# Performance work log

Hardware: AMD Instinct MI355X
Metric: run time of the kernel (lower is better)

## Reference

```python
import jax, jax.numpy as jnp
import numpy as np

B, H, L, DK = 8, 8, 512, 64
LK, C = 512, 5


def setup_inputs() -> dict:
    key = jax.random.key(0)
    ks = jax.random.split(key, 6)
    d_in = LK * H * DK  # l_k * d_model
    return {
        "Q": jax.random.normal(ks[0], (B, H, L, DK), dtype=jnp.float32),
        "K": jax.random.normal(ks[1], (B, H, LK, DK), dtype=jnp.float32),
        # scale by 1/sqrt(fan_in) so softmax inputs are sane
        "W_proj": jax.random.normal(ks[2], (d_in, C), dtype=jnp.float32) / np.sqrt(d_in),
        "b_proj": jnp.zeros((C,), dtype=jnp.float32),
        "W_q": jax.random.normal(ks[3], (C, C), dtype=jnp.float32) / np.sqrt(C),
        "b_q": jnp.zeros((C,), dtype=jnp.float32),
        "W_k": jax.random.normal(ks[4], (C, C), dtype=jnp.float32) / np.sqrt(C),
        "b_k": jnp.zeros((C,), dtype=jnp.float32),
    }


def reference(Q, K, W_proj, b_proj, W_q, b_q, W_k, b_k):
    b, h, l, d_k = Q.shape
    l_k = K.shape[2]
    n_clusters = b_proj.shape[0]
    hd = h * d_k

    # cluster projections over flattened K
    ck_proj = K.reshape(b, -1) @ W_proj + b_proj            # (b, C)
    cluster_q = jax.nn.softmax(ck_proj @ W_q + b_q, axis=-1)  # (b, C)
    cluster_k = jax.nn.softmax(ck_proj @ W_k + b_k, axis=-1)  # (b, C)

    # Gaussian likelihood term (torch.std is unbiased -> ddof=1)
    mu = jnp.mean(cluster_q, axis=0)                         # (C,)
    sigma = jax.nn.softplus(jnp.std(cluster_k, axis=0, ddof=1))
    log_prob = (-0.5 * ((cluster_k - mu) / sigma) ** 2
                - jnp.log(sigma) - 0.5 * jnp.log(2.0 * jnp.pi))
    # CrossEntropyLoss with prob targets: mean_b(-sum target*log_softmax(input))
    ce = jnp.mean(-jnp.sum(cluster_q * jax.nn.log_softmax(cluster_q, axis=-1), axis=-1))
    loss = -jnp.mean(log_prob) + ce

    # cluster assignment per batch element
    inds = jnp.argmax(cluster_q, axis=-1)                    # (b,) in [0, C)

    # The original per-cluster loop with where(K_cluster != i+1, K_inds, 0) then
    # mean(dim=0)[0] reduces to: mean over batch of K_re[:,0,:] masked where
    # assignment != i+1, broadcast across l_k.
    K_re = K.reshape(b, l_k, hd)
    row0 = K_re[:, 0, :]                                     # (b, hd)
    keep = (inds[None, :] != (jnp.arange(n_clusters) + 1)[:, None]).astype(Q.dtype)  # (C, b)
    means = (keep @ row0) / b                                # (C, hd)

    # broadcast to (b, C, l_k, hd) then raw reshape to (b, h, C, l_k, d_k)
    cm = jnp.broadcast_to(means[None, :, None, :], (b, n_clusters, l_k, hd))
    cm = cm.reshape(b, h, n_clusters, l_k, d_k)

    scale = 1.0 / np.sqrt(d_k)
    scores_qk = jnp.einsum('bhqd,bhkd->bhqk', Q, K) * scale          # (b,h,l,l_k)
    scores_qc = jnp.einsum('bhqd,bhckd->bhcqk', Q, cm) * scale       # (b,h,C,l,l_k)
    # max over cat([qk, qc], dim=2) == elementwise max of qk and max_c qc
    final_score = jnp.maximum(scores_qk, jnp.max(scores_qc, axis=2))
    return final_score, loss
```

## Files before the change

### kernel.cpp

```cpp
#include <hip/hip_runtime.h>
#include <math.h>

#define NB 8
#define NH 8
#define SEQ 512
#define DK 64
#define NC 5
#define D_IN 262144
#define OUT_SCORE (NB*NH*SEQ*SEQ)

typedef short short8 __attribute__((ext_vector_type(8)));
typedef float f32x16 __attribute__((ext_vector_type(16)));

__device__ __forceinline__ short f2bf(float f) {
  unsigned u = __float_as_uint(f);
  u += 0x7fffu + ((u >> 16) & 1u);
  return (short)(u >> 16);
}
__device__ __forceinline__ short8 pack8(float4 a, float4 b) {
  short8 r;
  r[0] = f2bf(a.x); r[1] = f2bf(a.y); r[2] = f2bf(a.z); r[3] = f2bf(a.w);
  r[4] = f2bf(b.x); r[5] = f2bf(b.y); r[6] = f2bf(b.z); r[7] = f2bf(b.w);
  return r;
}

__global__ __launch_bounds__(256) void proj_kernel(const float* __restrict__ K,
                                                   const float* __restrict__ Wp,
                                                   float* __restrict__ ck) {
  int i4 = blockIdx.x * 256 + threadIdx.x;
  const float4* Wp4 = (const float4*)Wp;
  float w[20];
#pragma unroll
  for (int t = 0; t < 5; ++t) {
    float4 v = Wp4[i4 * 5 + t];
    w[4*t+0] = v.x; w[4*t+1] = v.y; w[4*t+2] = v.z; w[4*t+3] = v.w;
  }
  float acc[NB][NC];
#pragma unroll
  for (int b = 0; b < NB; ++b)
#pragma unroll
    for (int c = 0; c < NC; ++c) acc[b][c] = 0.f;
#pragma unroll
  for (int b = 0; b < NB; ++b) {
    float4 kv = ((const float4*)(K + (size_t)b * D_IN))[i4];
    float ke[4] = {kv.x, kv.y, kv.z, kv.w};
#pragma unroll
    for (int e = 0; e < 4; ++e)
#pragma unroll
      for (int c = 0; c < NC; ++c)
        acc[b][c] = fmaf(ke[e], w[5*e + c], acc[b][c]);
  }

  __shared__ float red[4][NB * NC];
  int wave = threadIdx.x >> 6;
  int lane = threadIdx.x & 63;
#pragma unroll
  for (int bc = 0; bc < NB * NC; ++bc) {
    float v = acc[bc / NC][bc % NC];
#pragma unroll
    for (int off = 32; off > 0; off >>= 1) v += __shfl_down(v, off);
    if (lane == 0) red[wave][bc] = v;
  }
  __syncthreads();
  if (threadIdx.x < NB * NC) {
    float s = red[0][threadIdx.x] + red[1][threadIdx.x] +
              red[2][threadIdx.x] + red[3][threadIdx.x];
    atomicAdd(&ck[threadIdx.x], s);
  }
}

__global__ __launch_bounds__(256) void small_kernel(
    const float* __restrict__ K, const float* __restrict__ ck_raw,
    const float* __restrict__ bp, const float* __restrict__ Wq,
    const float* __restrict__ bq, const float* __restrict__ Wk,
    const float* __restrict__ bk, float* __restrict__ means,
    float* __restrict__ loss_out) {
  __shared__ float cq[NB][NC], ckk[NB][NC], ce_sh[NB];
  __shared__ int inds[NB];
  int t = threadIdx.x;
  if (t < NB) {
    float cp[NC], zq[NC], zk[NC];
#pragma unroll
    for (int c = 0; c < NC; ++c) cp[c] = ck_raw[t * NC + c] + bp[c];
#pragma unroll
    for (int c = 0; c < NC; ++c) { zq[c] = bq[c]; zk[c] = bk[c]; }
#pragma unroll
    for (int j = 0; j < NC; ++j)
#pragma unroll
      for (int c = 0; c < NC; ++c) {
        zq[c] = fmaf(cp[j], Wq[j * NC + c], zq[c]);
        zk[c] = fmaf(cp[j], Wk[j * NC + c], zk[c]);
      }
    float m = zq[0];
#pragma unroll
    for (int c = 1; c < NC; ++c) m = fmaxf(m, zq[c]);
    float e[NC], s = 0.f;
#pragma unroll
    for (int c = 0; c < NC; ++c) { e[c] = expf(zq[c] - m); s += e[c]; }
    float inv = 1.f / s;
    float p[NC];
#pragma unroll
    for (int c = 0; c < NC; ++c) { p[c] = e[c] * inv; cq[t][c] = p[c]; }
    int am = 0; float bv = p[0];
#pragma unroll
    for (int c = 1; c < NC; ++c) if (p[c] > bv) { bv = p[c]; am = c; }
    inds[t] = am;
    float se = 0.f;
#pragma unroll
    for (int c = 0; c < NC; ++c) se += expf(p[c] - bv);
    float lse = bv + logf(se);
    float ceb = 0.f;
#pragma unroll
    for (int c = 0; c < NC; ++c) ceb -= p[c] * (p[c] - lse);
    ce_sh[t] = ceb;
    m = zk[0];
#pragma unroll
    for (int c = 1; c < NC; ++c) m = fmaxf(m, zk[c]);
    s = 0.f;
#pragma unroll
    for (int c = 0; c < NC; ++c) { e[c] = expf(zk[c] - m); s += e[c]; }
    inv = 1.f / s;
#pragma unroll
    for (int c = 0; c < NC; ++c) ckk[t][c] = e[c] * inv;
  }
  __syncthreads();
  if (t == 0) {
    float mu[NC];
#pragma unroll
    for (int c = 0; c < NC; ++c) {
      float sm = 0.f;
      for (int b = 0; b < NB; ++b) sm += cq[b][c];
      mu[c] = sm * 0.125f;
    }
    float loss_lp = 0.f;
#pragma unroll
    for (int c = 0; c < NC; ++c) {
      float sm = 0.f;
      for (int b = 0; b < NB; ++b) sm += ckk[b][c];
      float mk = sm * 0.125f;
      float var = 0.f;
      for (int b = 0; b < NB; ++b) {
        float d = ckk[b][c] - mk;
        var += d * d;
      }
      var *= (1.f / 7.f);
      float sd = sqrtf(var);
      float sigma = log1pf(expf(sd));
      float ls = logf(sigma);
      for (int b = 0; b < NB; ++b) {
        float z = (ckk[b][c] - mu[c]) / sigma;
        loss_lp += -0.5f * z * z - ls - 0.91893853320467274f;
      }
    }
    float ce = 0.f;
    for (int b = 0; b < NB; ++b) ce += ce_sh[b];
    ce *= 0.125f;
    loss_out[0] = -(loss_lp / 40.f) + ce;
  }
  __syncthreads();
  for (int idx = t; idx < NC * 512; idx += 256) {
    int c = idx >> 9, j = idx & 511;
    float sm = 0.f;
#pragma unroll
    for (int b = 0; b < NB; ++b)
      if (inds[b] != c + 1) sm += K[(size_t)b * D_IN + j];
    means[idx] = sm * 0.125f;
  }
}

#define LDSTRIDE 72
__global__ __launch_bounds__(256) void score_kernel(const float* __restrict__ Q,
                                                    const float* __restrict__ K,
                                                    const float* __restrict__ means,
                                                    float* __restrict__ out) {
  __shared__ short Qs[128 * LDSTRIDE];
  __shared__ short Ks[128 * LDSTRIDE];

  const int bh = blockIdx.x;
  const int h  = bh & 7;
  const int qblk = blockIdx.y << 7;
  const int kblk = blockIdx.z << 7;
  const int tid = threadIdx.x;
  const int w = tid >> 6, lane = tid & 63;
  const int lo5 = lane & 31, hi = lane >> 5;
  const int wq = (w >> 1) << 6;
  const int wk = (w & 1) << 6;

  const float* Qg = Q + (size_t)bh * (SEQ * DK) + (size_t)qblk * DK;
  const float* Kg = K + (size_t)bh * (SEQ * DK) + (size_t)kblk * DK;

#pragma unroll
  for (int i = 0; i < 4; ++i) {
    int f8 = i * 256 + tid;
    int row = f8 >> 3, c8 = f8 & 7;
    const float4* qp = (const float4*)(Qg + row * DK + c8 * 8);
    const float4* kp = (const float4*)(Kg + row * DK + c8 * 8);
    *(short8*)&Qs[row * LDSTRIDE + c8 * 8] = pack8(qp[0], qp[1]);
    *(short8*)&Ks[row * LDSTRIDE + c8 * 8] = pack8(kp[0], kp[1]);
  }

  const int cmin = (5 * h) >> 3;
  const int cmax = (5 * h + 4) >> 3;
  short8 mfrag[4];
#pragma unroll
  for (int s = 0; s < 4; ++s) {
    float4 a = {0.f, 0.f, 0.f, 0.f}, b = {0.f, 0.f, 0.f, 0.f};
    if (lo5 < 16) {
      int c = (lo5 < 8) ? cmin : cmax;
      const float* mp = means + c * 512 + (lo5 & 7) * 64 + s * 16 + hi * 8;
      a = *(const float4*)mp;
      b = *(const float4*)(mp + 4);
    }
    mfrag[s] = pack8(a, b);
  }

  __syncthreads();

  f32x16 zero;
#pragma unroll
  for (int x = 0; x < 16; ++x) zero[x] = 0.f;

  f32x16 acc00 = zero, acc01 = zero, acc10 = zero, acc11 = zero;
  f32x16 aq0 = zero, aq1 = zero;
#pragma unroll
  for (int s = 0; s < 4; ++s) {
    int co = s * 16 + hi * 8;
    short8 a0 = *(const short8*)&Qs[(wq + lo5)      * LDSTRIDE + co];
    short8 a1 = *(const short8*)&Qs[(wq + 32 + lo5) * LDSTRIDE + co];
    short8 b0 = *(const short8*)&Ks[(wk + lo5)      * LDSTRIDE + co];
    short8 b1 = *(const short8*)&Ks[(wk + 32 + lo5) * LDSTRIDE + co];
    acc00 = __builtin_amdgcn_mfma_f32_32x32x16_bf16(a0, b0, acc00, 0, 0, 0);
    acc01 = __builtin_amdgcn_mfma_f32_32x32x16_bf16(a0, b1, acc01, 0, 0, 0);
    acc10 = __builtin_amdgcn_mfma_f32_32x32x16_bf16(a1, b0, acc10, 0, 0, 0);
    acc11 = __builtin_amdgcn_mfma_f32_32x32x16_bf16(a1, b1, acc11, 0, 0, 0);
    aq0   = __builtin_amdgcn_mfma_f32_32x32x16_bf16(a0, mfrag[s], aq0, 0, 0, 0);
    aq1   = __builtin_amdgcn_mfma_f32_32x32x16_bf16(a1, mfrag[s], aq1, 0, 0, 0);
  }

  float qcv0[16], qcv1[16];
  const int src0 = (hi << 5) + (lo5 & 7);
#pragma unroll
  for (int reg = 0; reg < 16; ++reg) {
    float m0 = fmaxf(__shfl(aq0[reg], src0), __shfl(aq0[reg], src0 + 8));
    float m1 = fmaxf(__shfl(aq1[reg], src0), __shfl(aq1[reg], src0 + 8));
    qcv0[reg] = m0 * 0.125f;
    qcv1[reg] = m1 * 0.125f;
  }

  float* ob = out + (size_t)bh * (SEQ * SEQ);
  const int kc0 = kblk + wk + lo5;
#pragma unroll
  for (int g = 0; g < 4; ++g) {
#pragma unroll
    for (int e = 0; e < 4; ++e) {
      int reg = 4 * g + e;
      int qrow = qblk + wq + e + 8 * g + 4 * hi;
      float q0 = qcv0[reg], q1 = qcv1[reg];
      __builtin_nontemporal_store(fmaxf(acc00[reg] * 0.125f, q0),
                                  ob + (size_t)qrow * SEQ + kc0);
      __builtin_nontemporal_store(fmaxf(acc01[reg] * 0.125f, q0),
                                  ob + (size_t)qrow * SEQ + kc0 + 32);
      __builtin_nontemporal_store(fmaxf(acc10[reg] * 0.125f, q1),
                                  ob + (size_t)(qrow + 32) * SEQ + kc0);
      __builtin_nontemporal_store(fmaxf(acc11[reg] * 0.125f, q1),
                                  ob + (size_t)(qrow + 32) * SEQ + kc0 + 32);
    }
  }
}

extern "C" void kernel_launch(void* const* d_in, const int* in_sizes, int n_in,
                              void* d_out, int out_size, void* d_ws, size_t ws_size,
                              hipStream_t stream) {
  const float* Q  = (const float*)d_in[0];
  const float* K  = (const float*)d_in[1];
  const float* Wp = (const float*)d_in[2];
  const float* bp = (const float*)d_in[3];
  const float* Wq = (const float*)d_in[4];
  const float* bq = (const float*)d_in[5];
  const float* Wk = (const float*)d_in[6];
  const float* bk = (const float*)d_in[7];
  float* out = (float*)d_out;

  float* ck = (float*)d_ws;
  float* means = ck + 64;

  hipMemsetAsync(ck, 0, NB * NC * sizeof(float), stream);
  proj_kernel<<<256, 256, 0, stream>>>(K, Wp, ck);
  small_kernel<<<1, 256, 0, stream>>>(K, ck, bp, Wq, bq, Wk, bk, means,
                                      out + OUT_SCORE);
  dim3 grid(64, 4, 4);
  score_kernel<<<grid, 256, 0, stream>>>(Q, K, means, out);
}
```

Measured before the change: 137.5 us.

## Replace atomics with per-block partials and reshuffle cluster-max via LDS

```diff
diff --git a/kernel.cpp b/kernel.cpp
--- a/kernel.cpp
+++ b/kernel.cpp
@@ -8,6 +8,7 @@
 #define NC 5
 #define D_IN 262144
 #define OUT_SCORE (NB*NH*SEQ*SEQ)
+#define PROJ_BLOCKS 128
 
 typedef short short8 __attribute__((ext_vector_type(8)));
 typedef float f32x16 __attribute__((ext_vector_type(16)));
@@ -26,29 +27,33 @@
 
 __global__ __launch_bounds__(256) void proj_kernel(const float* __restrict__ K,
                                                    const float* __restrict__ Wp,
-                                                   float* __restrict__ ck) {
-  int i4 = blockIdx.x * 256 + threadIdx.x;
+                                                   float* __restrict__ part) {
   const float4* Wp4 = (const float4*)Wp;
-  float w[20];
-#pragma unroll
-  for (int t = 0; t < 5; ++t) {
-    float4 v = Wp4[i4 * 5 + t];
-    w[4*t+0] = v.x; w[4*t+1] = v.y; w[4*t+2] = v.z; w[4*t+3] = v.w;
-  }
   float acc[NB][NC];
 #pragma unroll
   for (int b = 0; b < NB; ++b)
 #pragma unroll
     for (int c = 0; c < NC; ++c) acc[b][c] = 0.f;
-#pragma unroll
-  for (int b = 0; b < NB; ++b) {
-    float4 kv = ((const float4*)(K + (size_t)b * D_IN))[i4];
-    float ke[4] = {kv.x, kv.y, kv.z, kv.w};
-#pragma unroll
-    for (int e = 0; e < 4; ++e)
-#pragma unroll
-      for (int c = 0; c < NC; ++c)
-        acc[b][c] = fmaf(ke[e], w[5*e + c], acc[b][c]);
+
+#pragma unroll
+  for (int it = 0; it < 2; ++it) {
+    int i4 = blockIdx.x * 512 + it * 256 + threadIdx.x;
+    float w[20];
+#pragma unroll
+    for (int t = 0; t < 5; ++t) {
+      float4 v = Wp4[i4 * 5 + t];
+      w[4*t+0] = v.x; w[4*t+1] = v.y; w[4*t+2] = v.z; w[4*t+3] = v.w;
+    }
+#pragma unroll
+    for (int b = 0; b < NB; ++b) {
+      float4 kv = ((const float4*)(K + (size_t)b * D_IN))[i4];
+      float ke[4] = {kv.x, kv.y, kv.z, kv.w};
+#pragma unroll
+      for (int e = 0; e < 4; ++e)
+#pragma unroll
+        for (int c = 0; c < NC; ++c)
+          acc[b][c] = fmaf(ke[e], w[5*e + c], acc[b][c]);
+    }
   }
 
   __shared__ float red[4][NB * NC];
@@ -62,26 +67,32 @@
     if (lane == 0) red[wave][bc] = v;
   }
   __syncthreads();
-  if (threadIdx.x < NB * NC) {
-    float s = red[0][threadIdx.x] + red[1][threadIdx.x] +
-              red[2][threadIdx.x] + red[3][threadIdx.x];
-    atomicAdd(&ck[threadIdx.x], s);
-  }
+  if (threadIdx.x < NB * NC)
+    part[blockIdx.x * (NB * NC) + threadIdx.x] =
+        red[0][threadIdx.x] + red[1][threadIdx.x] +
+        red[2][threadIdx.x] + red[3][threadIdx.x];
 }
 
 __global__ __launch_bounds__(256) void small_kernel(
-    const float* __restrict__ K, const float* __restrict__ ck_raw,
+    const float* __restrict__ K, const float* __restrict__ part,
     const float* __restrict__ bp, const float* __restrict__ Wq,
     const float* __restrict__ bq, const float* __restrict__ Wk,
     const float* __restrict__ bk, float* __restrict__ means,
     float* __restrict__ loss_out) {
+  __shared__ float colsum[NB * NC];
   __shared__ float cq[NB][NC], ckk[NB][NC], ce_sh[NB];
   __shared__ int inds[NB];
   int t = threadIdx.x;
+  if (t < NB * NC) {
+    float s = 0.f;
+    for (int i = 0; i < PROJ_BLOCKS; ++i) s += part[i * (NB * NC) + t];
+    colsum[t] = s;
+  }
+  __syncthreads();
   if (t < NB) {
     float cp[NC], zq[NC], zk[NC];
 #pragma unroll
-    for (int c = 0; c < NC; ++c) cp[c] = ck_raw[t * NC + c] + bp[c];
+    for (int c = 0; c < NC; ++c) cp[c] = colsum[t * NC + c] + bp[c];
 #pragma unroll
     for (int c = 0; c < NC; ++c) { zq[c] = bq[c]; zk[c] = bk[c]; }
 #pragma unroll
@@ -175,6 +186,7 @@
                                                     float* __restrict__ out) {
   __shared__ short Qs[128 * LDSTRIDE];
   __shared__ short Ks[128 * LDSTRIDE];
+  __shared__ float qcbuf[4 * 64 * 10];
 
   const int bh = blockIdx.x;
   const int h  = bh & 7;
@@ -233,37 +245,45 @@
     acc01 = __builtin_amdgcn_mfma_f32_32x32x16_bf16(a0, b1, acc01, 0, 0, 0);
     acc10 = __builtin_amdgcn_mfma_f32_32x32x16_bf16(a1, b0, acc10, 0, 0, 0);
     acc11 = __builtin_amdgcn_mfma_f32_32x32x16_bf16(a1, b1, acc11, 0, 0, 0);
-    aq0   = __builtin_amdgcn_mfma_f32_32x32x16_bf16(a0, mfrag[s], aq0, 0, 0, 0);
-    aq1   = __builtin_amdgcn_mfma_f32_32x32x16_bf16(a1, mfrag[s], aq1, 0, 0, 0);
-  }
-
-  float qcv0[16], qcv1[16];
-  const int src0 = (hi << 5) + (lo5 & 7);
-#pragma unroll
-  for (int reg = 0; reg < 16; ++reg) {
-    float m0 = fmaxf(__shfl(aq0[reg], src0), __shfl(aq0[reg], src0 + 8));
-    float m1 = fmaxf(__shfl(aq1[reg], src0), __shfl(aq1[reg], src0 + 8));
-    qcv0[reg] = m0 * 0.125f;
-    qcv1[reg] = m1 * 0.125f;
+    aq0   = __builtin_amdgcn_mfma_f32_32x32x16_bf16(mfrag[s], a0, aq0, 0, 0, 0);
+    aq1   = __builtin_amdgcn_mfma_f32_32x32x16_bf16(mfrag[s], a1, aq1, 0, 0, 0);
+  }
+
+  {
+    int qb0 = w * 640 + lo5 * 10 + 4 * hi;
+    float2 p;
+    p.x = fmaxf(aq0[0], aq0[4]) * 0.125f;
+    p.y = fmaxf(aq0[1], aq0[5]) * 0.125f;
+    *(float2*)&qcbuf[qb0] = p;
+    p.x = fmaxf(aq0[2], aq0[6]) * 0.125f;
+    p.y = fmaxf(aq0[3], aq0[7]) * 0.125f;
+    *(float2*)&qcbuf[qb0 + 2] = p;
+    int qb1 = qb0 + 320;
+    p.x = fmaxf(aq1[0], aq1[4]) * 0.125f;
+    p.y = fmaxf(aq1[1], aq1[5]) * 0.125f;
+    *(float2*)&qcbuf[qb1] = p;
+    p.x = fmaxf(aq1[2], aq1[6]) * 0.125f;
+    p.y = fmaxf(aq1[3], aq1[7]) * 0.125f;
+    *(float2*)&qcbuf[qb1 + 2] = p;
   }
 
   float* ob = out + (size_t)bh * (SEQ * SEQ);
   const int kc0 = kblk + wk + lo5;
+  const int r = lo5 & 7;
+  const int qcb = w * 640 + r;
 #pragma unroll
   for (int g = 0; g < 4; ++g) {
 #pragma unroll
     for (int e = 0; e < 4; ++e) {
       int reg = 4 * g + e;
-      int qrow = qblk + wq + e + 8 * g + 4 * hi;
-      float q0 = qcv0[reg], q1 = qcv1[reg];
-      __builtin_nontemporal_store(fmaxf(acc00[reg] * 0.125f, q0),
-                                  ob + (size_t)qrow * SEQ + kc0);
-      __builtin_nontemporal_store(fmaxf(acc01[reg] * 0.125f, q0),
-                                  ob + (size_t)qrow * SEQ + kc0 + 32);
-      __builtin_nontemporal_store(fmaxf(acc10[reg] * 0.125f, q1),
-                                  ob + (size_t)(qrow + 32) * SEQ + kc0);
-      __builtin_nontemporal_store(fmaxf(acc11[reg] * 0.125f, q1),
-                                  ob + (size_t)(qrow + 32) * SEQ + kc0 + 32);
+      int ql = e + 8 * g + 4 * hi;
+      float qc0 = qcbuf[qcb + ql * 10];
+      float qc1 = qcbuf[qcb + (ql + 32) * 10];
+      int qrow = qblk + wq + ql;
+      ob[(size_t)qrow * SEQ + kc0]             = fmaxf(acc00[reg] * 0.125f, qc0);
+      ob[(size_t)qrow * SEQ + kc0 + 32]        = fmaxf(acc01[reg] * 0.125f, qc0);
+      ob[(size_t)(qrow + 32) * SEQ + kc0]      = fmaxf(acc10[reg] * 0.125f, qc1);
+      ob[(size_t)(qrow + 32) * SEQ + kc0 + 32] = fmaxf(acc11[reg] * 0.125f, qc1);
     }
   }
 }
@@ -281,12 +301,11 @@
   const float* bk = (const float*)d_in[7];
   float* out = (float*)d_out;
 
-  float* ck = (float*)d_ws;
-  float* means = ck + 64;
-
-  hipMemsetAsync(ck, 0, NB * NC * sizeof(float), stream);
-  proj_kernel<<<256, 256, 0, stream>>>(K, Wp, ck);
-  small_kernel<<<1, 256, 0, stream>>>(K, ck, bp, Wq, bq, Wk, bk, means,
+  float* part  = (float*)d_ws;
+  float* means = part + 8192;
+
+  proj_kernel<<<PROJ_BLOCKS, 256, 0, stream>>>(K, Wp, part);
+  small_kernel<<<1, 256, 0, stream>>>(K, part, bp, Wq, bq, Wk, bk, means,
                                       out + OUT_SCORE);
   dim3 grid(64, 4, 4);
   score_kernel<<<grid, 256, 0, stream>>>(Q, K, means, out);
```

Result: faster. 130.9 us (-4.8%).
